# Performance work log

Measured on AMD Instinct MI355X. Metric: run time of the kernel, lower is better.

Reference implementation:

```python
import jax, jax.numpy as jnp
import numpy as np

IN_C = 64
K = 3          # kernel_size
PAD = K // 2   # padding for offset_conv and deformconv


def conv2d(x, w, b, pad):
    # x: [B,C,H,W], w: [O,I,kh,kw] (OIHW), stride 1
    y = jax.lax.conv_general_dilated(
        x, w, (1, 1), [(pad, pad), (pad, pad)],
        dimension_numbers=('NCHW', 'OIHW', 'NCHW'))
    return y + b[None, :, None, None]


def deform_conv2d(x, offset, w, b, pad):
    # torchvision DeformConv2d (v1, no modulation), stride=1, dilation=1.
    # x: [B,Cin,H,W]; offset: [B,2*K*K,H,W] as (dy,dx) pairs per kernel tap
    # (row-major tap order); w: [Cout,Cin,K,K]; b: [Cout].
    B, Cin, H, W = x.shape
    Kh = w.shape[-1]
    K2 = Kh * Kh
    off = offset.reshape(B, K2, 2, H, W)
    dy, dx = off[:, :, 0], off[:, :, 1]                     # [B,K2,H,W]

    ky = (jnp.arange(K2) // Kh).astype(x.dtype)             # kernel tap rows
    kx = (jnp.arange(K2) % Kh).astype(x.dtype)              # kernel tap cols
    base_y = jnp.arange(H, dtype=x.dtype)[None, :, None] - pad + ky[:, None, None]  # [K2,H,1]
    base_x = jnp.arange(W, dtype=x.dtype)[None, None, :] - pad + kx[:, None, None]  # [K2,1,W]
    py = base_y[None] + dy                                  # [B,K2,H,W] sample y
    px = base_x[None] + dx                                  # [B,K2,H,W] sample x

    y0 = jnp.floor(py)
    x0 = jnp.floor(px)
    wy1 = py - y0; wy0 = 1.0 - wy1                          # bilinear weights
    wx1 = px - x0; wx0 = 1.0 - wx1

    x_flat = x.reshape(B, Cin, H * W)

    def gather(iy, ix):
        # zero-padded bilinear corner gather -> [B,Cin,K2,H,W]
        valid = (iy >= 0) & (iy < H) & (ix >= 0) & (ix < W)
        iyc = jnp.clip(iy, 0, H - 1).astype(jnp.int32)
        ixc = jnp.clip(ix, 0, W - 1).astype(jnp.int32)
        flat = (iyc * W + ixc).reshape(B, -1)               # [B,K2*H*W]
        g = jax.vmap(lambda xb, ib: xb[:, ib])(x_flat, flat)
        g = g.reshape(B, Cin, K2, H, W)
        return g * valid.reshape(B, 1, K2, H, W).astype(x.dtype)

    val = (gather(y0,       x0      ) * (wy0 * wx0)[:, None]
         + gather(y0,       x0 + 1.0) * (wy0 * wx1)[:, None]
         + gather(y0 + 1.0, x0      ) * (wy1 * wx0)[:, None]
         + gather(y0 + 1.0, x0 + 1.0) * (wy1 * wx1)[:, None])  # [B,Cin,K2,H,W]

    out = jnp.einsum('bckhw,ock->bohw', val, w.reshape(w.shape[0], Cin, K2))
    return out + b[None, :, None, None]


def setup_inputs() -> dict:
    key = jax.random.key(0)
    ks = jax.random.split(key, 7)
    B, H, W = 2, 256, 256
    f32 = jnp.float32
    x = jax.random.normal(ks[0], (B, IN_C, H, W), f32)
    # ConvTranspose2d weight layout: [in_c, out_c=64, K, K]
    w_deconv = jax.random.normal(ks[1], (IN_C, 64, K, K), f32) * 0.05
    b_deconv = jax.random.normal(ks[2], (64,), f32) * 0.05
    w_off = jax.random.normal(ks[3], (2 * K * K, 64, K, K), f32) * 0.05
    b_off = jax.random.normal(ks[4], (2 * K * K,), f32) * 0.05
    w_def = jax.random.normal(ks[5], (IN_C, 64, K, K), f32) * 0.05
    b_def = jax.random.normal(ks[6], (IN_C,), f32) * 0.05
    return {'x': x, 'w_deconv': w_deconv, 'b_deconv': b_deconv,
            'w_off': w_off, 'b_off': b_off, 'w_def': w_def, 'b_def': b_def}


def reference(x, w_deconv, b_deconv, w_off, b_off, w_def, b_def):
    # ConvTranspose2d(stride=1, pad=1) == conv with flipped, IO-transposed
    # weights and padding K-1-1 = 1.
    wt = jnp.flip(w_deconv, (2, 3)).transpose(1, 0, 2, 3)   # [64, in_c, K, K]
    h = jax.nn.relu(conv2d(x, wt, b_deconv, K - 1 - 1))
    offset = conv2d(h, w_off, b_off, PAD)
    out = deform_conv2d(h, offset, w_def, b_def, PAD)
    return jax.nn.relu(out)
```

## Files before the change

kernel.cpp:

```cpp
#include <hip/hip_runtime.h>

#define H_ 256
#define W_ 256
#define HW_ (H_*W_)

typedef __attribute__((ext_vector_type(8))) short bf16x8;
typedef __attribute__((ext_vector_type(4))) float f32x4;

__device__ __forceinline__ float bflo(unsigned u) { return __builtin_bit_cast(float, u << 16); }
__device__ __forceinline__ float bfhi(unsigned u) { return __builtin_bit_cast(float, u & 0xffff0000u); }
__device__ __forceinline__ unsigned f2bf(float f) {
    unsigned b = __builtin_bit_cast(unsigned, f);
    b += 0x7fffu + ((b >> 16) & 1u);
    return b >> 16;
}
__device__ __forceinline__ unsigned cvtpk(float lo, float hi) {
    unsigned r;
    asm("v_cvt_pk_bf16_f32 %0, %1, %2" : "=v"(r) : "v"(lo), "v"(hi));
    return r;
}
__device__ __forceinline__ void unpack8(uint4 v, float* f) {
    f[0] = bflo(v.x); f[1] = bfhi(v.x); f[2] = bflo(v.y); f[3] = bfhi(v.y);
    f[4] = bflo(v.z); f[5] = bfhi(v.z); f[6] = bflo(v.w); f[7] = bfhi(v.w);
}

__global__ void prep_weights(const float* __restrict__ wdef, unsigned short* __restrict__ wdefb,
                             const float* __restrict__ wdc, unsigned short* __restrict__ wdcb,
                             const float* __restrict__ woff, unsigned short* __restrict__ woffb) {
    int idx = blockIdx.x * 256 + threadIdx.x;
    if (idx < 36864) {
        int k = idx >> 12, o = (idx >> 6) & 63, c = idx & 63;
        wdefb[idx] = (unsigned short)f2bf(wdef[(o * 64 + c) * 9 + k]);
        wdcb[idx]  = (unsigned short)f2bf(wdc[(c * 64 + o) * 9 + (8 - k)]);
    }
    if (idx < 18432) {
        int k = idx >> 11, o = (idx >> 6) & 31, c = idx & 63;
        woffb[idx] = (o < 18) ? (unsigned short)f2bf(woff[(o * 64 + c) * 9 + k])
                              : (unsigned short)0;
    }
}

__global__ __launch_bounds__(256) void x_to_nhwc(const float* __restrict__ x,
                                                 unsigned short* __restrict__ xb) {
    __shared__ unsigned short t[64 * 72];
    int tid = threadIdx.x;
    int b = blockIdx.x >> 10;
    long pxb = (long)(blockIdx.x & 1023) * 64;
    const float* xp = x + (long)b * 64 * HW_ + pxb;
    int px = tid & 63, cg = tid >> 6;
    for (int c = cg; c < 64; c += 4)
        t[px * 72 + c] = (unsigned short)f2bf(xp[(long)c * HW_ + px]);
    __syncthreads();
    int spx = tid >> 2, q = tid & 3;
    unsigned short* dst = xb + ((long)b * HW_ + pxb + spx) * 64 + q * 16;
    *(uint4*)dst       = *(const uint4*)&t[spx * 72 + q * 16];
    *(uint4*)(dst + 8) = *(const uint4*)&t[spx * 72 + q * 16 + 8];
}

__global__ __launch_bounds__(256, 4) void conv1_mfma(const unsigned short* __restrict__ xb,
                                                     const unsigned short* __restrict__ wdcb,
                                                     const float* __restrict__ bias,
                                                     unsigned short* __restrict__ h) {
    __shared__ __align__(16) unsigned short sA[2][130 * 72];

    int tid = threadIdx.x;
    int linear = (blockIdx.x & 7) * 128 + (blockIdx.x >> 3);
    int bx = linear & 1;
    int y  = (linear >> 1) & 255;
    int b  = linear >> 9;
    int X0 = bx * 128;

    int wave = tid >> 6, lane = tid & 63;
    int lr = lane & 15, lg = lane >> 4;
    int n0 = wave * 16;

    f32x4 acc[8];
#pragma unroll
    for (int m = 0; m < 8; ++m) { acc[m][0]=0.f; acc[m][1]=0.f; acc[m][2]=0.f; acc[m][3]=0.f; }

    const unsigned short* xbb = xb + (long)b * HW_ * 64;
    const unsigned short* pb  = wdcb + (n0 + lr) * 64 + lg * 8;

    int r0 = (y == 0) ? 1 : 0;
    int r1 = (y == H_ - 1) ? 1 : 2;

    uint4 L[5];
    auto LOADROW = [&](int yr) {
        const unsigned short* src = xbb + (long)yr * (W_ * 64);
#pragma unroll
        for (int t = 0; t < 5; ++t) {
            int e = tid + t * 256;
            uint4 v = { 0u, 0u, 0u, 0u };
            if (e < 1040) {
                int col = X0 - 1 + (e >> 3);
                if (col >= 0 && col < W_)
                    v = *(const uint4*)&src[(long)col * 64 + (e & 7) * 8];
            }
            L[t] = v;
        }
    };

    LOADROW(y + r0 - 1);
    int pa = 0;
    for (int ky = r0; ky <= r1; ++ky, ++pa) {
        unsigned short* buf = sA[pa & 1];
#pragma unroll
        for (int t = 0; t < 5; ++t) {
            int e = tid + t * 256;
            if (e < 1040) *(uint4*)&buf[(e >> 3) * 72 + (e & 7) * 8] = L[t];
        }
        if (ky < r1) LOADROW(y + ky);
        asm volatile("s_waitcnt lgkmcnt(0)" ::: "memory");
        __builtin_amdgcn_s_barrier();
        asm volatile("" ::: "memory");
#pragma unroll
        for (int kx = 0; kx < 3; ++kx) {
            int k = ky * 3 + kx;
            bf16x8 b0 = *(const bf16x8*)(pb + k * 4096);
            bf16x8 b1 = *(const bf16x8*)(pb + k * 4096 + 32);
#pragma unroll
            for (int m = 0; m < 8; ++m) {
                const unsigned short* ap = &buf[(m * 16 + lr + kx) * 72 + lg * 8];
                bf16x8 a0 = *(const bf16x8*)ap;
                bf16x8 a1 = *(const bf16x8*)(ap + 32);
                acc[m] = __builtin_amdgcn_mfma_f32_16x16x32_bf16(a0, b0, acc[m], 0, 0, 0);
                acc[m] = __builtin_amdgcn_mfma_f32_16x16x32_bf16(a1, b1, acc[m], 0, 0, 0);
            }
        }
    }

    __syncthreads();
    float bv = bias[n0 + lr];
    unsigned short* cs = sA[0];
#pragma unroll
    for (int m = 0; m < 8; ++m)
#pragma unroll
        for (int r = 0; r < 4; ++r) {
            float vv = fmaxf(acc[m][r] + bv, 0.f);
            cs[(m * 16 + lg * 4 + r) * 72 + n0 + lr] = (unsigned short)f2bf(vv);
        }
    __syncthreads();
    int spx = tid >> 1, sc0 = (tid & 1) * 32;
    unsigned short* dst = h + ((long)b * HW_ + (long)y * W_ + X0 + spx) * 64 + sc0;
    const unsigned short* srcp = &cs[spx * 72 + sc0];
#pragma unroll
    for (int q = 0; q < 4; ++q)
        *(uint4*)(dst + q * 8) = *(const uint4*)(srcp + q * 8);
}

__global__ __launch_bounds__(256, 4) void conv2_mfma(const unsigned short* __restrict__ h,
                                                     const unsigned short* __restrict__ woffb,
                                                     const float* __restrict__ bias,
                                                     float* __restrict__ off) {
    __shared__ __align__(16) unsigned short sA[2][130 * 72];

    int tid = threadIdx.x;
    int linear = (blockIdx.x & 7) * 128 + (blockIdx.x >> 3);
    int bx = linear & 1;
    int y  = (linear >> 1) & 255;
    int b  = linear >> 9;
    int X0 = bx * 128;

    int wave = tid >> 6, lane = tid & 63;
    int lr = lane & 15, lg = lane >> 4;
    int pxh = wave & 1, nh = wave >> 1;
    int n0 = nh * 16;
    int pxb = pxh * 64;

    f32x4 acc[4];
#pragma unroll
    for (int m = 0; m < 4; ++m) { acc[m][0]=0.f; acc[m][1]=0.f; acc[m][2]=0.f; acc[m][3]=0.f; }

    const unsigned short* hb = h + (long)b * HW_ * 64;
    const unsigned short* pb = woffb + (n0 + lr) * 64 + lg * 8;

    int r0 = (y == 0) ? 1 : 0;
    int r1 = (y == H_ - 1) ? 1 : 2;

    uint4 L[5];
    auto LOADROW = [&](int yr) {
        const unsigned short* src = hb + (long)yr * (W_ * 64);
#pragma unroll
        for (int t = 0; t < 5; ++t) {
            int e = tid + t * 256;
            uint4 v = { 0u, 0u, 0u, 0u };
            if (e < 1040) {
                int col = X0 - 1 + (e >> 3);
                if (col >= 0 && col < W_)
                    v = *(const uint4*)&src[(long)col * 64 + (e & 7) * 8];
            }
            L[t] = v;
        }
    };

    LOADROW(y + r0 - 1);
    int pa = 0;
    for (int ky = r0; ky <= r1; ++ky, ++pa) {
        unsigned short* buf = sA[pa & 1];
#pragma unroll
        for (int t = 0; t < 5; ++t) {
            int e = tid + t * 256;
            if (e < 1040) *(uint4*)&buf[(e >> 3) * 72 + (e & 7) * 8] = L[t];
        }
        if (ky < r1) LOADROW(y + ky);
        asm volatile("s_waitcnt lgkmcnt(0)" ::: "memory");
        __builtin_amdgcn_s_barrier();
        asm volatile("" ::: "memory");
#pragma unroll
        for (int kx = 0; kx < 3; ++kx) {
            int k = ky * 3 + kx;
            bf16x8 b0 = *(const bf16x8*)(pb + k * 2048);
            bf16x8 b1 = *(const bf16x8*)(pb + k * 2048 + 32);
#pragma unroll
            for (int m = 0; m < 4; ++m) {
                const unsigned short* ap = &buf[(pxb + m * 16 + lr + kx) * 72 + lg * 8];
                bf16x8 a0 = *(const bf16x8*)ap;
                bf16x8 a1 = *(const bf16x8*)(ap + 32);
                acc[m] = __builtin_amdgcn_mfma_f32_16x16x32_bf16(a0, b0, acc[m], 0, 0, 0);
                acc[m] = __builtin_amdgcn_mfma_f32_16x16x32_bf16(a1, b1, acc[m], 0, 0, 0);
            }
        }
    }

    int o = n0 + lr;
    if (o < 18) {
        float bv = bias[o];
        float* op = off + ((long)b * 18 + o) * HW_ + (long)y * W_ + X0 + pxb;
#pragma unroll
        for (int m = 0; m < 4; ++m) {
            float4 r = { acc[m][0] + bv, acc[m][1] + bv, acc[m][2] + bv, acc[m][3] + bv };
            *(float4*)(op + m * 16 + lg * 4) = r;
        }
    }
}

struct Pass16 {
    uint4 a00, a01, a10, a11;
    uint4 b00, b01, b10, b11;
    float w00, w01, w10, w11;
};

__device__ __forceinline__ Pass16 issue16(const unsigned short* __restrict__ hb,
                                          int k, int y, int px, float dy, float dx, int c0) {
    Pass16 s;
    float py  = (float)(y - 1 + k / 3) + dy;
    float pxs = (float)(px - 1 + k % 3) + dx;
    float y0f = floorf(py), x0f = floorf(pxs);
    int iy0 = (int)y0f, ix0 = (int)x0f;
    float wy1 = py - y0f, wx1 = pxs - x0f;
    float wy0 = 1.f - wy1, wx0 = 1.f - wx1;
    bool vy0 = (iy0 >= 0) && (iy0 < H_);
    bool vy1 = (iy0 >= -1) && (iy0 < H_ - 1);
    bool vx0 = (ix0 >= 0) && (ix0 < W_);
    bool vx1 = (ix0 >= -1) && (ix0 < W_ - 1);
    int cy0 = min(max(iy0, 0), H_ - 1), cy1 = min(max(iy0 + 1, 0), H_ - 1);
    int cx0 = min(max(ix0, 0), W_ - 1), cx1 = min(max(ix0 + 1, 0), W_ - 1);
    s.w00 = wy0 * wx0 * ((vy0 && vx0) ? 1.f : 0.f);
    s.w01 = wy0 * wx1 * ((vy0 && vx1) ? 1.f : 0.f);
    s.w10 = wy1 * wx0 * ((vy1 && vx0) ? 1.f : 0.f);
    s.w11 = wy1 * wx1 * ((vy1 && vx1) ? 1.f : 0.f);
    int r00 = (cy0 * W_ + cx0) * 64 + c0, r01 = (cy0 * W_ + cx1) * 64 + c0;
    int r10 = (cy1 * W_ + cx0) * 64 + c0, r11 = (cy1 * W_ + cx1) * 64 + c0;
    s.a00 = *(const uint4*)&hb[r00];     s.a01 = *(const uint4*)&hb[r01];
    s.a10 = *(const uint4*)&hb[r10];     s.a11 = *(const uint4*)&hb[r11];
    s.b00 = *(const uint4*)&hb[r00 + 8]; s.b01 = *(const uint4*)&hb[r01 + 8];
    s.b10 = *(const uint4*)&hb[r10 + 8]; s.b11 = *(const uint4*)&hb[r11 + 8];
    return s;
}

__device__ __forceinline__ uint4 interp8u(uint4 q0, uint4 q1, uint4 q2, uint4 q3,
                                          float w00, float w01, float w10, float w11) {
    float g0[8], g1[8], g2[8], g3[8];
    unpack8(q0, g0); unpack8(q1, g1); unpack8(q2, g2); unpack8(q3, g3);
    unsigned r[4];
#pragma unroll
    for (int j = 0; j < 4; ++j) {
        float lo = fmaf(g3[2*j],   w11, fmaf(g2[2*j],   w10, fmaf(g1[2*j],   w01, g0[2*j]   * w00)));
        float hi = fmaf(g3[2*j+1], w11, fmaf(g2[2*j+1], w10, fmaf(g1[2*j+1], w01, g0[2*j+1] * w00)));
        r[j] = cvtpk(lo, hi);
    }
    uint4 u = { r[0], r[1], r[2], r[3] };
    return u;
}

__global__ __launch_bounds__(256, 4) void deform_mfma(const unsigned short* __restrict__ h,
                                                      const float* __restrict__ off,
                                                      const unsigned short* __restrict__ wdefb,
                                                      const float* __restrict__ bias,
                                                      float* __restrict__ out) {
    __shared__ __align__(16) unsigned short val[2][64 * 64];

    int tid = threadIdx.x;
    int linear = (blockIdx.x & 7) * 256 + (blockIdx.x >> 3);
    int b  = linear >> 10;
    int y  = (linear >> 2) & 255;
    int x0 = (linear & 3) * 64;

    int lane = tid & 63, wave = tid >> 6;
    int lr = lane & 15, lg = lane >> 4;
    int n0 = wave * 16;
    int gpx = tid >> 2;
    int gc  = tid & 3;
    int c0  = gc * 16;
    int gx  = x0 + gpx;

    f32x4 acc[4];
#pragma unroll
    for (int m = 0; m < 4; ++m) { acc[m][0]=0.f; acc[m][1]=0.f; acc[m][2]=0.f; acc[m][3]=0.f; }

    const unsigned short* hb   = h + (long)b * HW_ * 64;
    const float* ofb  = off + (long)b * 18 * HW_ + y * W_ + gx;
    const unsigned short* bsrc = wdefb + (n0 + lr) * 64 + lg * 8;

    float dy0 = ofb[0], dx0 = ofb[HW_];
    Pass16 S = issue16(hb, 0, y, gx, dy0, dx0, c0);
    float dyn = ofb[2 * HW_], dxn = ofb[3 * HW_];
    bf16x8 bc0 = *(const bf16x8*)bsrc;
    bf16x8 bc1 = *(const bf16x8*)(bsrc + 32);

    int slotL = ((2 * gc)     ^ (gpx & 7)) * 8;
    int slotH = ((2 * gc + 1) ^ (gpx & 7)) * 8;
    int rdL   = ((lg)     ^ (lr & 7)) * 8;
    int rdH   = ((lg + 4) ^ (lr & 7)) * 8;

#pragma unroll
    for (int k = 0; k < 9; ++k) {
        Pass16 S2;
        bf16x8 bn0 = bc0, bn1 = bc1;
        float dy3 = 0.f, dx3 = 0.f;
        if (k < 8) {
            S2  = issue16(hb, k + 1, y, gx, dyn, dxn, c0);
            bn0 = *(const bf16x8*)(bsrc + (k + 1) * 4096);
            bn1 = *(const bf16x8*)(bsrc + (k + 1) * 4096 + 32);
            if (k < 7) { dy3 = ofb[(2 * k + 4) * HW_]; dx3 = ofb[(2 * k + 5) * HW_]; }
        }

        unsigned short* vb = val[k & 1];
        *(uint4*)&vb[gpx * 64 + slotL] = interp8u(S.a00, S.a01, S.a10, S.a11,
                                                  S.w00, S.w01, S.w10, S.w11);
        *(uint4*)&vb[gpx * 64 + slotH] = interp8u(S.b00, S.b01, S.b10, S.b11,
                                                  S.w00, S.w01, S.w10, S.w11);

        asm volatile("s_waitcnt lgkmcnt(0)" ::: "memory");
        __builtin_amdgcn_s_barrier();
        asm volatile("" ::: "memory");

        __builtin_amdgcn_s_setprio(1);
#pragma unroll
        for (int m = 0; m < 4; ++m) {
            const unsigned short* ap = &vb[(m * 16 + lr) * 64];
            bf16x8 a0 = *(const bf16x8*)&ap[rdL];
            bf16x8 a1 = *(const bf16x8*)&ap[rdH];
            acc[m] = __builtin_amdgcn_mfma_f32_16x16x32_bf16(a0, bc0, acc[m], 0, 0, 0);
            acc[m] = __builtin_amdgcn_mfma_f32_16x16x32_bf16(a1, bc1, acc[m], 0, 0, 0);
        }
        __builtin_amdgcn_s_setprio(0);

        S = S2; bc0 = bn0; bc1 = bn1; dyn = dy3; dxn = dx3;
    }

    float bv = bias[n0 + lr];
    float* outb = out + ((long)b * 64 + n0 + lr) * HW_ + y * W_ + x0;
#pragma unroll
    for (int m = 0; m < 4; ++m) {
        float4 r = { fmaxf(acc[m][0] + bv, 0.f), fmaxf(acc[m][1] + bv, 0.f),
                     fmaxf(acc[m][2] + bv, 0.f), fmaxf(acc[m][3] + bv, 0.f) };
        *(float4*)(outb + m * 16 + lg * 4) = r;
    }
}

extern "C" void kernel_launch(void* const* d_in, const int* in_sizes, int n_in,
                              void* d_out, int out_size, void* d_ws, size_t ws_size,
                              hipStream_t stream) {
    const float* x        = (const float*)d_in[0];
    const float* w_deconv = (const float*)d_in[1];
    const float* b_deconv = (const float*)d_in[2];
    const float* w_off    = (const float*)d_in[3];
    const float* b_off    = (const float*)d_in[4];
    const float* w_def    = (const float*)d_in[5];
    const float* b_def    = (const float*)d_in[6];
    float* out = (float*)d_out;

    char* ws = (char*)d_ws;
    unsigned short* xbb   = (unsigned short*)ws;
    unsigned short* hbf   = (unsigned short*)(ws + 16777216);
    float* offset         = (float*)(ws + 33554432);
    unsigned short* wdcb  = (unsigned short*)(ws + 42991616);
    unsigned short* wdefb = (unsigned short*)(ws + 43065344);
    unsigned short* woffb = (unsigned short*)(ws + 43139072);

    prep_weights<<<144, 256, 0, stream>>>(w_def, wdefb, w_deconv, wdcb, w_off, woffb);
    x_to_nhwc<<<2048, 256, 0, stream>>>(x, xbb);
    conv1_mfma<<<1024, 256, 0, stream>>>(xbb, wdcb, b_deconv, hbf);
    conv2_mfma<<<1024, 256, 0, stream>>>(hbf, woffb, b_off, offset);
    deform_mfma<<<2048, 256, 0, stream>>>(hbf, offset, wdefb, b_def, out);
}
```

Measured before the change: 113.5 us.

## Make each wave own its pixel slice to drop block-wide barrier in deform conv

Reworks the deformable-conv MFMA kernel so each wave interpolates and consumes its own 16 pixels across all 64 output channels, instead of sharing 64 pixels block-wide and splitting output channels across waves. This replaces the per-tap __syncthreads-style s_barrier with a wave-local LDS wait and a scheduling barrier, removing cross-wave synchronisation. Weights for all four output groups are now loaded from global each tap rather than prefetched, which raises register pressure (launch bounds lowered to 3 blocks per SM). The k loop is no longer explicitly unrolled.

```diff
diff --git a/kernel.cpp b/kernel.cpp
--- a/kernel.cpp
+++ b/kernel.cpp
@@ -283,12 +283,12 @@
     return u;
 }
 
-__global__ __launch_bounds__(256, 4) void deform_mfma(const unsigned short* __restrict__ h,
+__global__ __launch_bounds__(256, 3) void deform_mfma(const unsigned short* __restrict__ h,
                                                       const float* __restrict__ off,
                                                       const unsigned short* __restrict__ wdefb,
                                                       const float* __restrict__ bias,
                                                       float* __restrict__ out) {
-    __shared__ __align__(16) unsigned short val[2][64 * 64];
+    __shared__ __align__(16) unsigned short val[2][4][16 * 64];
 
     int tid = threadIdx.x;
     int linear = (blockIdx.x & 7) * 256 + (blockIdx.x >> 3);
@@ -298,74 +298,69 @@
 
     int lane = tid & 63, wave = tid >> 6;
     int lr = lane & 15, lg = lane >> 4;
-    int n0 = wave * 16;
-    int gpx = tid >> 2;
-    int gc  = tid & 3;
+    int wpx0 = x0 + wave * 16;
+    int gpx = lane >> 2;
+    int gc  = lane & 3;
     int c0  = gc * 16;
-    int gx  = x0 + gpx;
+    int gx  = wpx0 + gpx;
 
     f32x4 acc[4];
 #pragma unroll
     for (int m = 0; m < 4; ++m) { acc[m][0]=0.f; acc[m][1]=0.f; acc[m][2]=0.f; acc[m][3]=0.f; }
 
-    const unsigned short* hb   = h + (long)b * HW_ * 64;
-    const float* ofb  = off + (long)b * 18 * HW_ + y * W_ + gx;
-    const unsigned short* bsrc = wdefb + (n0 + lr) * 64 + lg * 8;
+    const unsigned short* hb = h + (long)b * HW_ * 64;
+    const float* ofb = off + (long)b * 18 * HW_ + y * W_ + gx;
 
     float dy0 = ofb[0], dx0 = ofb[HW_];
     Pass16 S = issue16(hb, 0, y, gx, dy0, dx0, c0);
     float dyn = ofb[2 * HW_], dxn = ofb[3 * HW_];
-    bf16x8 bc0 = *(const bf16x8*)bsrc;
-    bf16x8 bc1 = *(const bf16x8*)(bsrc + 32);
 
     int slotL = ((2 * gc)     ^ (gpx & 7)) * 8;
     int slotH = ((2 * gc + 1) ^ (gpx & 7)) * 8;
     int rdL   = ((lg)     ^ (lr & 7)) * 8;
-    int rdH   = ((lg + 4) ^ (lr & 7)) * 8;
-
-#pragma unroll
+    int rdH   = ((4 + lg) ^ (lr & 7)) * 8;
+
     for (int k = 0; k < 9; ++k) {
+        const unsigned short* wk = wdefb + k * 4096 + lr * 64 + lg * 8;
+        bf16x8 Wf[8];
+#pragma unroll
+        for (int og = 0; og < 4; ++og) {
+            Wf[og * 2]     = *(const bf16x8*)(wk + og * 1024);
+            Wf[og * 2 + 1] = *(const bf16x8*)(wk + og * 1024 + 32);
+        }
         Pass16 S2;
-        bf16x8 bn0 = bc0, bn1 = bc1;
         float dy3 = 0.f, dx3 = 0.f;
         if (k < 8) {
-            S2  = issue16(hb, k + 1, y, gx, dyn, dxn, c0);
-            bn0 = *(const bf16x8*)(bsrc + (k + 1) * 4096);
-            bn1 = *(const bf16x8*)(bsrc + (k + 1) * 4096 + 32);
+            S2 = issue16(hb, k + 1, y, gx, dyn, dxn, c0);
             if (k < 7) { dy3 = ofb[(2 * k + 4) * HW_]; dx3 = ofb[(2 * k + 5) * HW_]; }
         }
-
-        unsigned short* vb = val[k & 1];
+        unsigned short* vb = &val[k & 1][wave][0];
         *(uint4*)&vb[gpx * 64 + slotL] = interp8u(S.a00, S.a01, S.a10, S.a11,
                                                   S.w00, S.w01, S.w10, S.w11);
         *(uint4*)&vb[gpx * 64 + slotH] = interp8u(S.b00, S.b01, S.b10, S.b11,
                                                   S.w00, S.w01, S.w10, S.w11);
-
         asm volatile("s_waitcnt lgkmcnt(0)" ::: "memory");
-        __builtin_amdgcn_s_barrier();
-        asm volatile("" ::: "memory");
-
+        __builtin_amdgcn_sched_barrier(0);
+        bf16x8 a0 = *(const bf16x8*)&vb[lr * 64 + rdL];
+        bf16x8 a1 = *(const bf16x8*)&vb[lr * 64 + rdH];
         __builtin_amdgcn_s_setprio(1);
 #pragma unroll
-        for (int m = 0; m < 4; ++m) {
-            const unsigned short* ap = &vb[(m * 16 + lr) * 64];
-            bf16x8 a0 = *(const bf16x8*)&ap[rdL];
-            bf16x8 a1 = *(const bf16x8*)&ap[rdH];
-            acc[m] = __builtin_amdgcn_mfma_f32_16x16x32_bf16(a0, bc0, acc[m], 0, 0, 0);
-            acc[m] = __builtin_amdgcn_mfma_f32_16x16x32_bf16(a1, bc1, acc[m], 0, 0, 0);
+        for (int og = 0; og < 4; ++og) {
+            acc[og] = __builtin_amdgcn_mfma_f32_16x16x32_bf16(a0, Wf[og * 2],     acc[og], 0, 0, 0);
+            acc[og] = __builtin_amdgcn_mfma_f32_16x16x32_bf16(a1, Wf[og * 2 + 1], acc[og], 0, 0, 0);
         }
         __builtin_amdgcn_s_setprio(0);
 
-        S = S2; bc0 = bn0; bc1 = bn1; dyn = dy3; dxn = dx3;
-    }
-
-    float bv = bias[n0 + lr];
-    float* outb = out + ((long)b * 64 + n0 + lr) * HW_ + y * W_ + x0;
-#pragma unroll
-    for (int m = 0; m < 4; ++m) {
-        float4 r = { fmaxf(acc[m][0] + bv, 0.f), fmaxf(acc[m][1] + bv, 0.f),
-                     fmaxf(acc[m][2] + bv, 0.f), fmaxf(acc[m][3] + bv, 0.f) };
-        *(float4*)(outb + m * 16 + lg * 4) = r;
+        S = S2; dyn = dy3; dxn = dx3;
+    }
+
+    float* outb = out + (long)b * 64 * HW_ + (long)y * W_ + wpx0;
+#pragma unroll
+    for (int og = 0; og < 4; ++og) {
+        float bv = bias[og * 16 + lr];
+        float4 r = { fmaxf(acc[og][0] + bv, 0.f), fmaxf(acc[og][1] + bv, 0.f),
+                     fmaxf(acc[og][2] + bv, 0.f), fmaxf(acc[og][3] + bv, 0.f) };
+        *(float4*)(outb + (long)(og * 16 + lr) * HW_ + lg * 4) = r;
     }
 }
 
```

Result: slower. 140.3 us (+23.6%).
